# Kernel optimization log

Hardware: AMD Instinct MI355X
Metric: run time of the kernel (lower is better)

The kernel has to match this reference:

```python
import jax, jax.numpy as jnp
import numpy as np

WAVEFORM_TICKS = 512
BIN_SIGMA = 5.0
NX, NY = 48, 48
GAUSS_NORM = 0.3989422804  # 1/sqrt(2*pi)
EL_NORM = 2.5066           # sqrt(2*pi) as hard-coded in the module
B, NE = 4, 5000
H1, H2 = 64, 128


def setup_inputs() -> dict:
    key = jax.random.key(0)
    ks = jax.random.split(key, 8)
    simulator_input = 0.5 * jax.random.normal(ks[0], (B, NE, 2), dtype=jnp.float32)
    z_positions = jax.random.uniform(ks[1], (B, NE), dtype=jnp.float32) * (WAVEFORM_TICKS - 1)
    mask = jax.random.uniform(ks[2], (B, NE), dtype=jnp.float32)
    # MLP params: 2 -> 64 -> 128 -> 1
    W1 = jax.random.normal(ks[3], (2, H1), dtype=jnp.float32) * (1.0 / np.sqrt(2.0))
    b1 = jnp.zeros((H1,), jnp.float32)
    W2 = jax.random.normal(ks[4], (H1, H2), dtype=jnp.float32) * (1.0 / np.sqrt(H1))
    b2 = jnp.zeros((H2,), jnp.float32)
    W3 = jax.random.normal(ks[5], (H2, 1), dtype=jnp.float32) * (1.0 / np.sqrt(H2))
    b3 = jnp.zeros((1,), jnp.float32)
    # learned EL spread scalar, init 0.1 as in the module
    el_spread = 0.1 * jnp.ones((1,), jnp.float32)
    # SiPM grid locations in [-1, 1]^2 -> (NX, NY, 2)
    ax = jnp.linspace(-1.0, 1.0, NX, dtype=jnp.float32)
    ay = jnp.linspace(-1.0, 1.0, NY, dtype=jnp.float32)
    gx, gy = jnp.meshgrid(ax, ay, indexing='ij')
    sensor_locations = jnp.stack([gx, gy], axis=-1)
    return {"simulator_input": simulator_input, "z_positions": z_positions, "mask": mask,
            "W1": W1, "b1": b1, "W2": W2, "b2": b2, "W3": W3, "b3": b3,
            "el_spread": el_spread, "sensor_locations": sensor_locations}


def reference(simulator_input, z_positions, mask, W1, b1, W2, b2, W3, b3, el_spread, sensor_locations):
    # MLP per-electron light yield: (B, NE, 2) -> (B, NE)
    h = jax.nn.relu(simulator_input @ W1 + b1)
    h = jax.nn.relu(h @ W2 + b2)
    response = (h @ W3 + b3)[..., 0]

    # spatial gaussian spread onto the sensor grid: (B, NE, NX, NY)
    diff = simulator_input[:, :, None, None, :] - sensor_locations  # (B,NE,NX,NY,2)
    r_squared = jnp.sum(diff * diff, axis=-1)
    es = el_spread[0]
    sipm_spread = 100.0 * jnp.exp(-0.5 * r_squared / (es * es)) / (es * EL_NORM)
    sensor_response = sipm_spread * response[:, :, None, None]  # (B,NE,NX,NY)

    # time-domain gaussian binning: (B, NE, T)
    t = jnp.arange(WAVEFORM_TICKS, dtype=simulator_input.dtype)
    ev = jnp.exp(-((t[None, None, :] - z_positions[..., None]) ** 2) / (2.0 * BIN_SIGMA))
    ev = ev * (GAUSS_NORM / np.sqrt(BIN_SIGMA))
    ev = ev * mask[..., None]

    # contract over electrons: (B,T,NE) x (B,NE,NX*NY) -> (B,T,NX*NY)
    sens_flat = sensor_response.reshape(B, NE, NX * NY)
    wf = jnp.einsum('bet,bes->bts', ev, sens_flat)
    wf = wf.reshape(B, WAVEFORM_TICKS, NX, NY).transpose(0, 2, 3, 1)  # (B,NX,NY,T)
    return wf.sum(axis=0)  # (NX, NY, T)
```

## Files before the change

### kernel.cpp

```cpp
#include <hip/hip_runtime.h>
#include <math.h>

#define NXg 48
#define NYg 48
#define Tg 512
#define NG 20000
#define H1g 64
#define H2g 128

#define TT 32
#define NBINS 16
#define RCAP 3072
#define CCAP (RCAP / 32)
#define NSB 18

#define KSCALE 0.84932180028802f

typedef float vf16 __attribute__((ext_vector_type(16)));
typedef _Float16 half8 __attribute__((ext_vector_type(8)));
typedef float floatx4 __attribute__((ext_vector_type(4)));

#define OFF_BFRAG  0
#define OFF_POSC   (OFF_BFRAG  + (size_t)NBINS*CCAP*4*512*2)
#define OFF_EDATA2 (OFF_POSC   + (size_t)NBINS*RCAP*8)
#define OFF_LIST   (OFF_EDATA2 + (size_t)NG*16)
#define OFF_CNT    (OFF_LIST   + (size_t)NBINS*RCAP*4)

__global__ __launch_bounds__(256) void k_fused(
    const float* __restrict__ sim, const float* __restrict__ zpos,
    const float* __restrict__ mask,
    const float* __restrict__ W1, const float* __restrict__ b1,
    const float* __restrict__ W2, const float* __restrict__ b2,
    const float* __restrict__ W3, const float* __restrict__ b3,
    const float* __restrict__ el_spread,
    float4* __restrict__ edata2, int* __restrict__ cnt, int* __restrict__ list)
{
    __shared__ __align__(16) float sW2[H1g][H2g];
    __shared__ float4 sW1b[H1g];
    __shared__ int lcnt[NBINS], lbase[NBINS];

    int tid = threadIdx.x;
    if (tid < H1g)
        sW1b[tid] = make_float4(W1[tid], W1[H1g + tid], b1[tid], 0.0f);
    if (tid < NBINS) lcnt[tid] = 0;
    {
        float4* d = (float4*)&sW2[0][0];
        const float4* s = (const float4*)W2;
        for (int i = tid; i < H1g * H2g / 4; i += 256) d[i] = s[i];
    }
    __syncthreads();

    int sub = tid & 7;
    int g = blockIdx.x * 32 + (tid >> 3);
    int k0 = sub * 16;

    float2 s0 = *(const float2*)&sim[2 * g];

    vf16 a = *(const vf16*)&b2[k0];
#pragma unroll 4
    for (int j = 0; j < H1g; ++j) {
        float4 wb = sW1b[j];
        float h = fmaxf(fmaf(s0.x, wb.x, fmaf(s0.y, wb.y, wb.z)), 0.0f);
        vf16 w = *(const vf16*)&sW2[j][k0];
#pragma unroll
        for (int u = 0; u < 16; ++u) a[u] = fmaf(h, w[u], a[u]);
    }
    float r = (sub == 0) ? b3[0] : 0.0f;
#pragma unroll
    for (int u = 0; u < 16; ++u)
        r = fmaf(fmaxf(a[u], 0.0f), W3[k0 + u], r);
    r += __shfl_xor(r, 1);
    r += __shfl_xor(r, 2);
    r += __shfl_xor(r, 4);

    int jlo = 0, jhi = -1;
    int off[3];
    if (sub == 0) {
        float z = zpos[g];
        float es = el_spread[0];
        float amp = r * mask[g] * (100.0f / (es * 2.5066f)) *
                    (0.3989422804f / 2.23606797749979f);
        float kk = KSCALE / es;
        edata2[g] = make_float4(s0.x * kk, s0.y * kk, z, amp);
        jlo = max((int)ceilf((z - 44.5f) * (1.0f / 32.0f)), 0);
        jhi = min((int)floorf((z + 13.5f) * (1.0f / 32.0f)), NBINS - 1);
        for (int j = jlo; j <= jhi; ++j)
            off[j - jlo] = atomicAdd(&lcnt[j], 1);
    }
    __syncthreads();
    if (tid < NBINS) {
        int c = lcnt[tid];
        lbase[tid] = c ? atomicAdd(&cnt[tid], c) : 0;
    }
    __syncthreads();
    if (sub == 0) {
        for (int j = jlo; j <= jhi; ++j) {
            int p = lbase[j] + off[j - jlo];
            if (p < RCAP) list[j * RCAP + p] = g;
        }
    }
}

__global__ __launch_bounds__(256) void k_prof(
    const float4* __restrict__ edata2, const int* __restrict__ cnt,
    const int* __restrict__ list,
    _Float16* __restrict__ bfrag, float2* __restrict__ posc)
{
    __shared__ float4 sE[64];
    int bin = blockIdx.y;
    int tid = threadIdx.x;
    int count = min(cnt[bin], RCAP);
    int nch = (count + 31) >> 5;
    int cbase = blockIdx.x * 2;
    if (cbase >= nch) return;

    if (tid < 64) {
        int i = cbase * 32 + tid;
        float4 E = make_float4(1.0e3f, 1.0e3f, 0.0f, 0.0f);
        if (i < count) E = edata2[list[bin * RCAP + i]];
        sE[tid] = E;
        if (i < nch * 32)
            posc[(size_t)bin * RCAP + i] = make_float2(E.x, E.y);
    }
    __syncthreads();

    int ch = cbase + (tid >> 7);
    if (ch >= nch) return;
    int nt = (tid >> 6) & 1;
    int lane = tid & 63;
    int quad = lane >> 4, t16 = lane & 15;
    float tt = (float)(bin * TT + nt * 16 + t16);

    half8 hi, lo;
#pragma unroll
    for (int j = 0; j < 8; ++j) {
        float4 E = sE[(tid >> 7) * 32 + quad * 8 + j];
        float d = tt - E.z;
        float v = E.w * __expf(-0.1f * d * d);
        _Float16 h = (_Float16)v;
        hi[j] = h;
        lo[j] = (_Float16)(v - (float)h);
    }
    size_t base = ((size_t)(bin * CCAP + ch)) * 4 * 512;
    *(half8*)&bfrag[base + (size_t)nt * 512 + lane * 8] = hi;
    *(half8*)&bfrag[base + (size_t)(2 + nt) * 512 + lane * 8] = lo;
}

__global__ __launch_bounds__(256) void k_main(
    const _Float16* __restrict__ bfrag, const float2* __restrict__ posc,
    const int* __restrict__ cnt, const float* __restrict__ el_spread,
    const float* __restrict__ sensors, float* __restrict__ out)
{
    __shared__ float4 sPos[CCAP * 16];

    int tid = threadIdx.x;
    int wv = tid >> 6, lane = tid & 63;
    int sb = blockIdx.x, bin = blockIdx.y;
    int quad = lane >> 4;

    int count = min(cnt[bin], RCAP);
    int nch = (count + 31) >> 5;

    {
        const float4* psrc = (const float4*)(posc + (size_t)bin * RCAP);
        for (int i = tid; i < nch * 16; i += 256) sPos[i] = psrc[i];
    }
    __syncthreads();

    int sA = sb * 128 + wv * 32 + (lane & 15);
    float es = el_spread[0];
    float kk = KSCALE / es;
    float sx0 = sensors[2 * sA] * kk,        sy0 = sensors[2 * sA + 1] * kk;
    float sx1 = sensors[2 * (sA + 16)] * kk, sy1 = sensors[2 * (sA + 16) + 1] * kk;

    floatx4 d00 = {0.f,0.f,0.f,0.f}, d01 = {0.f,0.f,0.f,0.f};
    floatx4 d10 = {0.f,0.f,0.f,0.f}, d11 = {0.f,0.f,0.f,0.f};

    const half8* bbase = (const half8*)bfrag + (size_t)bin * CCAP * 256 + lane;
    const float4* lbase = sPos + quad * 4;

#define LOADC(c, F0, F1, F2, F3, Q0, Q1, Q2, Q3)                          \
    {                                                                     \
        const half8* bb = bbase + (size_t)(c) * 256;                      \
        F0 = bb[0]; F1 = bb[64]; F2 = bb[128]; F3 = bb[192];              \
        const float4* lp = lbase + (c) * 16;                              \
        Q0 = lp[0]; Q1 = lp[1]; Q2 = lp[2]; Q3 = lp[3];                   \
    }

#define COMP(F0, F1, F2, F3, Q0, Q1, Q2, Q3)                              \
    {                                                                     \
        float exs[8] = {Q0.x, Q0.z, Q1.x, Q1.z, Q2.x, Q2.z, Q3.x, Q3.z};  \
        float eys[8] = {Q0.y, Q0.w, Q1.y, Q1.w, Q2.y, Q2.w, Q3.y, Q3.w};  \
        half8 ah0, ah1;                                                   \
        _Pragma("unroll")                                                 \
        for (int j = 0; j < 8; ++j) {                                     \
            float dx0 = sx0 - exs[j], dy0 = sy0 - eys[j];                 \
            float dx1 = sx1 - exs[j], dy1 = sy1 - eys[j];                 \
            float e0 = __builtin_amdgcn_exp2f(-fmaf(dy0, dy0, dx0 * dx0));\
            float e1 = __builtin_amdgcn_exp2f(-fmaf(dy1, dy1, dx1 * dx1));\
            ah0[j] = (_Float16)e0;                                        \
            ah1[j] = (_Float16)e1;                                        \
        }                                                                 \
        d00 = __builtin_amdgcn_mfma_f32_16x16x32_f16(ah0, F0, d00, 0,0,0);\
        d01 = __builtin_amdgcn_mfma_f32_16x16x32_f16(ah0, F1, d01, 0,0,0);\
        d10 = __builtin_amdgcn_mfma_f32_16x16x32_f16(ah1, F0, d10, 0,0,0);\
        d11 = __builtin_amdgcn_mfma_f32_16x16x32_f16(ah1, F1, d11, 0,0,0);\
        d00 = __builtin_amdgcn_mfma_f32_16x16x32_f16(ah0, F2, d00, 0,0,0);\
        d01 = __builtin_amdgcn_mfma_f32_16x16x32_f16(ah0, F3, d01, 0,0,0);\
        d10 = __builtin_amdgcn_mfma_f32_16x16x32_f16(ah1, F2, d10, 0,0,0);\
        d11 = __builtin_amdgcn_mfma_f32_16x16x32_f16(ah1, F3, d11, 0,0,0);\
    }

    if (nch > 0) {
        half8 fA0, fA1, fA2, fA3, fB0, fB1, fB2, fB3;
        float4 qA0, qA1, qA2, qA3, qB0, qB1, qB2, qB3;
        LOADC(0, fA0, fA1, fA2, fA3, qA0, qA1, qA2, qA3);
        int c = 0;
        for (; c + 1 < nch; c += 2) {
            LOADC(c + 1, fB0, fB1, fB2, fB3, qB0, qB1, qB2, qB3);
            COMP(fA0, fA1, fA2, fA3, qA0, qA1, qA2, qA3);
            int cn = (c + 2 < nch) ? c + 2 : nch - 1;
            LOADC(cn, fA0, fA1, fA2, fA3, qA0, qA1, qA2, qA3);
            COMP(fB0, fB1, fB2, fB3, qB0, qB1, qB2, qB3);
        }
        if (c < nch) COMP(fA0, fA1, fA2, fA3, qA0, qA1, qA2, qA3);
    }
#undef LOADC
#undef COMP

    int n0 = lane & 15;
    int s0r = sb * 128 + wv * 32 + quad * 4;
#pragma unroll
    for (int r = 0; r < 4; ++r) {
        float* o0 = out + (size_t)(s0r + r) * Tg + bin * TT;
        o0[n0]      = d00[r];
        o0[16 + n0] = d01[r];
        float* o1 = o0 + 16 * Tg;
        o1[n0]      = d10[r];
        o1[16 + n0] = d11[r];
    }
}

extern "C" void kernel_launch(void* const* d_in, const int* in_sizes, int n_in,
                              void* d_out, int out_size, void* d_ws, size_t ws_size,
                              hipStream_t stream)
{
    const float* sim       = (const float*)d_in[0];
    const float* zpos      = (const float*)d_in[1];
    const float* mask      = (const float*)d_in[2];
    const float* W1        = (const float*)d_in[3];
    const float* b1        = (const float*)d_in[4];
    const float* W2        = (const float*)d_in[5];
    const float* b2        = (const float*)d_in[6];
    const float* W3        = (const float*)d_in[7];
    const float* b3        = (const float*)d_in[8];
    const float* el_spread = (const float*)d_in[9];
    const float* sensors   = (const float*)d_in[10];
    float* out = (float*)d_out;

    char* ws = (char*)d_ws;
    _Float16* bfrag  = (_Float16*)(ws + OFF_BFRAG);
    float2*   posc   = (float2*)(ws + OFF_POSC);
    float4*   edata2 = (float4*)(ws + OFF_EDATA2);
    int*      list   = (int*)(ws + OFF_LIST);
    int*      cnt    = (int*)(ws + OFF_CNT);

    hipMemsetAsync(cnt, 0, NBINS * sizeof(int), stream);

    k_fused<<<NG / 32, 256, 0, stream>>>(
        sim, zpos, mask, W1, b1, W2, b2, W3, b3, el_spread,
        edata2, cnt, list);

    k_prof<<<dim3(CCAP / 2, NBINS), 256, 0, stream>>>(
        edata2, cnt, list, bfrag, posc);

    k_main<<<dim3(NSB, NBINS), 256, 0, stream>>>(
        bfrag, posc, cnt, el_spread, sensors, out);
}
```

Baseline: 137.8 us.

## Split electron-chunk reduction in main kernel across three blocks with partial-sum reduce

Adds a third grid dimension to the main MFMA kernel, so each (sensor-block, time-bin) tile processes only a third of its electron chunks. Each block writes its partial accumulators to a workspace buffer, and a new reduce kernel sums the three partials into the output. This raises the block count from 288 to 864, which is meant to fix the poor occupancy and load balance of 288 blocks on a 256-CU device. In exchange it adds an extra kernel launch and partial-buffer global traffic, and it shrinks the shared-memory staging buffer to one split's worth of positions.

```diff
diff --git a/kernel.cpp b/kernel.cpp
--- a/kernel.cpp
+++ b/kernel.cpp
@@ -12,6 +12,7 @@
 #define NBINS 16
 #define RCAP 3072
 #define CCAP (RCAP / 32)
+#define SPLIT 3
 #define NSB 18
 
 #define KSCALE 0.84932180028802f
@@ -22,7 +23,8 @@
 
 #define OFF_BFRAG  0
 #define OFF_POSC   (OFF_BFRAG  + (size_t)NBINS*CCAP*4*512*2)
-#define OFF_EDATA2 (OFF_POSC   + (size_t)NBINS*RCAP*8)
+#define OFF_PART   (OFF_POSC   + (size_t)NBINS*RCAP*8)
+#define OFF_EDATA2 (OFF_PART   + (size_t)SPLIT*NSB*NBINS*4096*4)
 #define OFF_LIST   (OFF_EDATA2 + (size_t)NG*16)
 #define OFF_CNT    (OFF_LIST   + (size_t)NBINS*RCAP*4)
 
@@ -149,21 +151,23 @@
 __global__ __launch_bounds__(256) void k_main(
     const _Float16* __restrict__ bfrag, const float2* __restrict__ posc,
     const int* __restrict__ cnt, const float* __restrict__ el_spread,
-    const float* __restrict__ sensors, float* __restrict__ out)
-{
-    __shared__ float4 sPos[CCAP * 16];
+    const float* __restrict__ sensors, float* __restrict__ part)
+{
+    __shared__ float4 sPos[512];
 
     int tid = threadIdx.x;
     int wv = tid >> 6, lane = tid & 63;
-    int sb = blockIdx.x, bin = blockIdx.y;
+    int sb = blockIdx.x, bin = blockIdx.y, split = blockIdx.z;
     int quad = lane >> 4;
 
     int count = min(cnt[bin], RCAP);
     int nch = (count + 31) >> 5;
+    int c0 = nch * split / SPLIT, c1 = nch * (split + 1) / SPLIT;
+    int nc = c1 - c0;
 
     {
-        const float4* psrc = (const float4*)(posc + (size_t)bin * RCAP);
-        for (int i = tid; i < nch * 16; i += 256) sPos[i] = psrc[i];
+        const float4* psrc = (const float4*)(posc + (size_t)bin * RCAP + c0 * 32);
+        for (int i = tid; i < nc * 16; i += 256) sPos[i] = psrc[i];
     }
     __syncthreads();
 
@@ -183,7 +187,7 @@
     {                                                                     \
         const half8* bb = bbase + (size_t)(c) * 256;                      \
         F0 = bb[0]; F1 = bb[64]; F2 = bb[128]; F3 = bb[192];              \
-        const float4* lp = lbase + (c) * 16;                              \
+        const float4* lp = lbase + ((c) - c0) * 16;                       \
         Q0 = lp[0]; Q1 = lp[1]; Q2 = lp[2]; Q3 = lp[3];                   \
     }
 
@@ -211,33 +215,51 @@
         d11 = __builtin_amdgcn_mfma_f32_16x16x32_f16(ah1, F3, d11, 0,0,0);\
     }
 
-    if (nch > 0) {
+    if (c0 < c1) {
         half8 fA0, fA1, fA2, fA3, fB0, fB1, fB2, fB3;
         float4 qA0, qA1, qA2, qA3, qB0, qB1, qB2, qB3;
-        LOADC(0, fA0, fA1, fA2, fA3, qA0, qA1, qA2, qA3);
-        int c = 0;
-        for (; c + 1 < nch; c += 2) {
+        LOADC(c0, fA0, fA1, fA2, fA3, qA0, qA1, qA2, qA3);
+        int c = c0;
+        for (; c + 1 < c1; c += 2) {
             LOADC(c + 1, fB0, fB1, fB2, fB3, qB0, qB1, qB2, qB3);
             COMP(fA0, fA1, fA2, fA3, qA0, qA1, qA2, qA3);
-            int cn = (c + 2 < nch) ? c + 2 : nch - 1;
+            int cn = (c + 2 < c1) ? c + 2 : c1 - 1;
             LOADC(cn, fA0, fA1, fA2, fA3, qA0, qA1, qA2, qA3);
             COMP(fB0, fB1, fB2, fB3, qB0, qB1, qB2, qB3);
         }
-        if (c < nch) COMP(fA0, fA1, fA2, fA3, qA0, qA1, qA2, qA3);
+        if (c < c1) COMP(fA0, fA1, fA2, fA3, qA0, qA1, qA2, qA3);
     }
 #undef LOADC
 #undef COMP
 
+    float* pb = part + (((size_t)split * NSB + sb) * NBINS + bin) * 4096;
     int n0 = lane & 15;
-    int s0r = sb * 128 + wv * 32 + quad * 4;
 #pragma unroll
     for (int r = 0; r < 4; ++r) {
-        float* o0 = out + (size_t)(s0r + r) * Tg + bin * TT;
-        o0[n0]      = d00[r];
-        o0[16 + n0] = d01[r];
-        float* o1 = o0 + 16 * Tg;
-        o1[n0]      = d10[r];
-        o1[16 + n0] = d11[r];
+        int sl0 = wv * 32 + quad * 4 + r;
+        int sl1 = sl0 + 16;
+        pb[sl0 * 32 + n0]      = d00[r];
+        pb[sl0 * 32 + 16 + n0] = d01[r];
+        pb[sl1 * 32 + n0]      = d10[r];
+        pb[sl1 * 32 + 16 + n0] = d11[r];
+    }
+}
+
+__global__ __launch_bounds__(256) void k_reduce(
+    const float4* __restrict__ part, float* __restrict__ out)
+{
+    int sb = blockIdx.x, bin = blockIdx.y, tid = threadIdx.x;
+#pragma unroll
+    for (int h = 0; h < 4; ++h) {
+        int p = h * 256 + tid;
+        int sl = p >> 3, q = p & 7;
+        float4 s = make_float4(0.f, 0.f, 0.f, 0.f);
+        for (int sp = 0; sp < SPLIT; ++sp) {
+            float4 v = part[(((size_t)sp * NSB + sb) * NBINS + bin) * 1024 + p];
+            s.x += v.x; s.y += v.y; s.z += v.z; s.w += v.w;
+        }
+        int sensor = sb * 128 + sl;
+        *(float4*)(out + (size_t)sensor * Tg + bin * TT + q * 4) = s;
     }
 }
 
@@ -261,6 +283,7 @@
     char* ws = (char*)d_ws;
     _Float16* bfrag  = (_Float16*)(ws + OFF_BFRAG);
     float2*   posc   = (float2*)(ws + OFF_POSC);
+    float*    part   = (float*)(ws + OFF_PART);
     float4*   edata2 = (float4*)(ws + OFF_EDATA2);
     int*      list   = (int*)(ws + OFF_LIST);
     int*      cnt    = (int*)(ws + OFF_CNT);
@@ -274,6 +297,8 @@
     k_prof<<<dim3(CCAP / 2, NBINS), 256, 0, stream>>>(
         edata2, cnt, list, bfrag, posc);
 
-    k_main<<<dim3(NSB, NBINS), 256, 0, stream>>>(
-        bfrag, posc, cnt, el_spread, sensors, out);
-}
+    k_main<<<dim3(NSB, NBINS, SPLIT), 256, 0, stream>>>(
+        bfrag, posc, cnt, el_spread, sensors, part);
+
+    k_reduce<<<dim3(NSB, NBINS), 256, 0, stream>>>((const float4*)part, out);
+}
```

Measured after the change: 129.6 us. 5.9% less time.
